# Optimization experiments

Hardware: AMD Instinct MI355X
Metric: run time of the kernel (lower is better)

## Reference

```python
import jax, jax.numpy as jnp
import numpy as np


def _isotonic_nonincreasing(y):
    """argmin_{v1>=...>=vn} ||v - y||^2 (PAV solution) via the exact min-max
    formula v[i] = min_{j<=i} max_{k>=i} mean(y[j:k+1]), vectorized O(n^2)."""
    n = y.shape[0]
    S = jnp.concatenate([jnp.zeros(1, y.dtype), jnp.cumsum(y)])  # prefix sums, [n+1]
    j = jnp.arange(n)[:, None]
    k = jnp.arange(n)[None, :]
    den = (k - j + 1).astype(y.dtype)
    # A[j,k] = mean(y[j:k+1]); entries with k<j are never read (see masking argument below)
    A = (S[k + 1] - S[j]) / jnp.where(den > 0, den, jnp.ones((), y.dtype))
    # Mrev[j,i] = max_{k'>=i} A[j,k']; for queries i>=j only valid entries participate
    Mrev = jnp.flip(jax.lax.cummax(jnp.flip(A, 1), axis=1), 1)
    # C[i,i] = min_{j<=i} Mrev[j,i]
    C = jax.lax.cummin(Mrev, axis=0)
    return jnp.diagonal(C)


def _soft_rank_row(z):
    """torchsort.soft_rank (l2 regularization, ascending) on a 1-D vector:
    projection of z onto the permutahedron of (1..n)."""
    n = z.shape[0]
    perm = jnp.argsort(-z)                # descending sort
    s = z[perm]
    w = jnp.arange(n, 0, -1).astype(z.dtype)   # rho = [n, n-1, ..., 1]
    dual = _isotonic_nonincreasing(s - w)
    primal = s - dual
    return jnp.zeros_like(z).at[perm].set(primal)  # undo the sort


def soft_rank(x, regularization_strength=1.0):
    # x: [rows, n]; rank each row over its last dim
    return jax.vmap(_soft_rank_row)(x / regularization_strength)


def setup_inputs() -> dict:
    key = jax.random.key(0)
    ks = jax.random.split(key, 7)
    B, D_IN, H, D_OUT = 4096, 512, 2048, 1

    def lin(kw, kb, fan_in, fan_out):
        lim = 1.0 / np.sqrt(fan_in)  # torch nn.Linear default init
        W = jax.random.uniform(kw, (fan_in, fan_out), jnp.float32, -lim, lim)
        b = jax.random.uniform(kb, (fan_out,), jnp.float32, -lim, lim)
        return W, b

    x = jax.random.normal(ks[0], (B, D_IN), jnp.float32)
    W1, b1 = lin(ks[1], ks[2], D_IN, H)
    W2, b2 = lin(ks[3], ks[4], H, H)
    W3, b3 = lin(ks[5], ks[6], H, D_OUT)
    return {"x": x, "W1": W1, "b1": b1, "W2": W2, "b2": b2, "W3": W3, "b3": b3}


def reference(x, W1, b1, W2, b2, W3, b3):
    # fc stack; Dropout is identity in eval mode
    h = jax.nn.relu(x @ W1 + b1)
    h = jax.nn.relu(h @ W2 + b2)
    scores = h @ W3 + b3                       # [B, D_OUT]
    rank = soft_rank(scores.T, 1.0)            # [D_OUT, B], ranks across the batch
    return rank, scores
```

## Files before the change

### kernel.cpp

```cpp
#include <hip/hip_runtime.h>
#include <hip/hip_bf16.h>

typedef float f32x4 __attribute__((ext_vector_type(4)));
typedef __bf16 bf16x8 __attribute__((ext_vector_type(8)));

#define AS3(p) ((__attribute__((address_space(3))) void*)(p))
#define AS1(p) ((const __attribute__((address_space(1))) void*)(p))

__device__ __forceinline__ unsigned short f2bf(float f) {
    unsigned u = __float_as_uint(f);
    return (unsigned short)((u + 0x7fffu + ((u >> 16) & 1u)) >> 16);
}

__device__ __forceinline__ unsigned long long sort_key(float v, int idx) {
    unsigned ub = __float_as_uint(v);
    unsigned m  = (ub & 0x80000000u) ? ~ub : (ub | 0x80000000u);
    return ((unsigned long long)(~m) << 12) | (unsigned)idx;
}

__global__ __launch_bounds__(256) void prep_all(
    const float* __restrict__ x, unsigned short* __restrict__ xb,
    const float* __restrict__ W1, unsigned short* __restrict__ W1t,
    const float* __restrict__ W2, unsigned short* __restrict__ W2t,
    float* __restrict__ sc, int* __restrict__ posg)
{
    __shared__ float tile[64][65];
    const int bx = blockIdx.x;
    const int t = threadIdx.x;

    if (bx < 1024) {
        int i = bx * 2048 + t * 8;
        float4 v0 = *(const float4*)(x + i);
        float4 v1 = *(const float4*)(x + i + 4);
        ushort4 o0 = { f2bf(v0.x), f2bf(v0.y), f2bf(v0.z), f2bf(v0.w) };
        ushort4 o1 = { f2bf(v1.x), f2bf(v1.y), f2bf(v1.z), f2bf(v1.w) };
        *(ushort4*)(xb + i)     = o0;
        *(ushort4*)(xb + i + 4) = o1;
        return;
    }
    if (bx == 2304) {
        float4 z = {0.f, 0.f, 0.f, 0.f};
        int4 zi = {0, 0, 0, 0};
        #pragma unroll
        for (int i = 0; i < 4; ++i) {
            *(float4*)(sc + t * 16 + i * 4)  = z;
            *(int4*)(posg + t * 16 + i * 4)  = zi;
        }
        return;
    }
    int idx = bx - 1024;
    int ty = idx >> 5;
    int txi = idx & 31;
    const float* W; unsigned short* Wt; int K, N, by;
    if (ty < 8) { W = W1; Wt = W1t; K = 512;  N = 2048; by = ty; }
    else        { W = W2; Wt = W2t; K = 2048; N = 2048; by = ty - 8; }

    const int col4 = t & 15;
    const int row  = t >> 4;
    #pragma unroll
    for (int i = 0; i < 4; ++i) {
        int r = row + i * 16;
        float4 v = *(const float4*)(W + (size_t)(by * 64 + r) * N + txi * 64 + col4 * 4);
        tile[r][col4 * 4 + 0] = v.x;
        tile[r][col4 * 4 + 1] = v.y;
        tile[r][col4 * 4 + 2] = v.z;
        tile[r][col4 * 4 + 3] = v.w;
    }
    __syncthreads();
    #pragma unroll
    for (int i = 0; i < 4; ++i) {
        int r = row + i * 16;
        ushort4 o = { f2bf(tile[col4 * 4 + 0][r]), f2bf(tile[col4 * 4 + 1][r]),
                      f2bf(tile[col4 * 4 + 2][r]), f2bf(tile[col4 * 4 + 3][r]) };
        *(ushort4*)(Wt + (size_t)(txi * 64 + r) * K + by * 64 + col4 * 4) = o;
    }
}

#define GB_WAITV(n) { asm volatile("s_waitcnt vmcnt(" #n ")" ::: "memory"); \
                      __builtin_amdgcn_sched_barrier(0); }

template <int MODE>
__global__ __launch_bounds__(512, 2) void gemm_bf16_mfma(
    const unsigned short* __restrict__ A, const unsigned short* __restrict__ Bt,
    const float* __restrict__ bias, unsigned short* __restrict__ Cbf,
    const float* __restrict__ w3, float* __restrict__ scores,
    int M, int N, int K)
{
    __shared__ __align__(16) unsigned short lds3[3][384 * 64];
    constexpr int BOFF = 256 * 64;

    const int tid = threadIdx.x;
    const int wave = tid >> 6, lane = tid & 63;

    const unsigned nwg = gridDim.x * gridDim.y;
    const unsigned bid = blockIdx.y * gridDim.x + blockIdx.x;
    const unsigned sbid = (bid & 7u) * (nwg >> 3) + (bid >> 3);
    const int bn = sbid % gridDim.x;
    const int bm = sbid / gridDim.x;

    const int wm = (wave >> 1) * 64;
    const int wn = (wave & 1) * 64;

    const unsigned short* Ablk = A  + (size_t)(bm * 256) * K;
    const unsigned short* Bblk = Bt + (size_t)(bn * 128) * K;

    const int lc  = lane & 15;
    const int rl4 = lane >> 4;
    const int srow = lane >> 3;
    const int sgc  = ((lane & 7) ^ srow) << 3;

    f32x4 acc[4][4] = {};
    const int nt = K >> 6;

    unsigned short *Ac = lds3[0], *An = lds3[1], *Asp = lds3[2];

    #define STG_P1(k0, D) {                                                    \
        _Pragma("unroll")                                                      \
        for (int i = 0; i < 2; ++i) {                                          \
            const int ra = wave * 32 + i * 8 + srow;                           \
            __builtin_amdgcn_global_load_lds(                                  \
                AS1(Ablk + (size_t)ra * K + (k0) + sgc),                       \
                AS3((D) + (wave * 32 + i * 8) * 64), 16, 0, 0);                \
        }                                                                      \
        {                                                                      \
            const int rb = wave * 16 + srow;                                   \
            __builtin_amdgcn_global_load_lds(                                  \
                AS1(Bblk + (size_t)rb * K + (k0) + sgc),                       \
                AS3((D) + BOFF + (wave * 16) * 64), 16, 0, 0);                 \
        } }
    #define STG_P2(k0, D) {                                                    \
        _Pragma("unroll")                                                      \
        for (int i = 2; i < 4; ++i) {                                          \
            const int ra = wave * 32 + i * 8 + srow;                           \
            __builtin_amdgcn_global_load_lds(                                  \
                AS1(Ablk + (size_t)ra * K + (k0) + sgc),                       \
                AS3((D) + (wave * 32 + i * 8) * 64), 16, 0, 0);                \
        }                                                                      \
        {                                                                      \
            const int rb = wave * 16 + 8 + srow;                               \
            __builtin_amdgcn_global_load_lds(                                  \
                AS1(Bblk + (size_t)rb * K + (k0) + sgc),                       \
                AS3((D) + BOFF + (wave * 16 + 8) * 64), 16, 0, 0);             \
        } }

    STG_P1(0, Ac);  STG_P2(0, Ac);
    STG_P1(64, An); STG_P2(64, An);

    for (int t = 0; t < nt; ++t) {
        if (t < nt - 1) { GB_WAITV(6); } else { GB_WAITV(0); }
        __builtin_amdgcn_s_barrier();

        const bool pf = (t + 2 < nt);
        const int kpf = (t + 2) << 6;

        if (pf) STG_P1(kpf, Asp);
        bf16x8 a[4][2], b[2][2];
        #pragma unroll
        for (int mt = 0; mt < 4; ++mt)
            #pragma unroll
            for (int kk = 0; kk < 2; ++kk)
                a[mt][kk] = *(const bf16x8*)(
                    Ac + (wm + mt * 16 + lc) * 64 + (((kk * 4 + rl4) ^ (lc & 7)) << 3));
        #pragma unroll
        for (int n2 = 0; n2 < 2; ++n2)
            #pragma unroll
            for (int kk = 0; kk < 2; ++kk)
                b[n2][kk] = *(const bf16x8*)(
                    Ac + BOFF + (wn + n2 * 16 + lc) * 64 + (((kk * 4 + rl4) ^ (lc & 7)) << 3));
        __builtin_amdgcn_s_setprio(1);
        #pragma unroll
        for (int mt = 0; mt < 4; ++mt)
            #pragma unroll
            for (int n2 = 0; n2 < 2; ++n2)
                #pragma unroll
                for (int kk = 0; kk < 2; ++kk)
                    acc[mt][n2] = __builtin_amdgcn_mfma_f32_16x16x32_bf16(
                        a[mt][kk], b[n2][kk], acc[mt][n2], 0, 0, 0);
        __builtin_amdgcn_s_setprio(0);

        if (pf) STG_P2(kpf, Asp);
        #pragma unroll
        for (int n2 = 0; n2 < 2; ++n2)
            #pragma unroll
            for (int kk = 0; kk < 2; ++kk)
                b[n2][kk] = *(const bf16x8*)(
                    Ac + BOFF + (wn + 32 + n2 * 16 + lc) * 64 + (((kk * 4 + rl4) ^ (lc & 7)) << 3));
        __builtin_amdgcn_s_setprio(1);
        #pragma unroll
        for (int mt = 0; mt < 4; ++mt)
            #pragma unroll
            for (int n2 = 0; n2 < 2; ++n2)
                #pragma unroll
                for (int kk = 0; kk < 2; ++kk)
                    acc[mt][2 + n2] = __builtin_amdgcn_mfma_f32_16x16x32_bf16(
                        a[mt][kk], b[n2][kk], acc[mt][2 + n2], 0, 0, 0);
        __builtin_amdgcn_s_setprio(0);

        unsigned short* tmp = Ac; Ac = An; An = Asp; Asp = tmp;
    }

    #undef STG_P1
    #undef STG_P2

    const int cm0 = bm * 256 + wm;
    const int cn0 = bn * 128 + wn;
    const int lr = (lane >> 4) * 4;

    if (MODE == 0) {
        #pragma unroll
        for (int j = 0; j < 4; ++j) {
            float bv = bias[cn0 + j * 16 + lc];
            #pragma unroll
            for (int mt = 0; mt < 4; ++mt)
                #pragma unroll
                for (int r = 0; r < 4; ++r) {
                    float v = fmaxf(acc[mt][j][r] + bv, 0.0f);
                    size_t idx = (size_t)(cm0 + mt * 16 + lr + r) * N + cn0 + j * 16 + lc;
                    Cbf[idx] = f2bf(v);
                }
        }
    } else {
        float bv[4], w3v[4];
        #pragma unroll
        for (int j = 0; j < 4; ++j) {
            bv[j]  = bias[cn0 + j * 16 + lc];
            w3v[j] = w3[cn0 + j * 16 + lc];
        }
        #pragma unroll
        for (int mt = 0; mt < 4; ++mt)
            #pragma unroll
            for (int r = 0; r < 4; ++r) {
                float p = 0.0f;
                #pragma unroll
                for (int j = 0; j < 4; ++j)
                    p += fmaxf(acc[mt][j][r] + bv[j], 0.0f) * w3v[j];
                p += __shfl_xor(p, 1);
                p += __shfl_xor(p, 2);
                p += __shfl_xor(p, 4);
                p += __shfl_xor(p, 8);
                if (lc == 0)
                    atomicAdd(&scores[cm0 + mt * 16 + lr + r], p);
            }
    }
}

__global__ __launch_bounds__(256) void rank_count(
    const float* __restrict__ sc, const float* __restrict__ b3,
    float* __restrict__ out_scores, int* __restrict__ posg)
{
    __shared__ unsigned long long kj[256];
    const int t = threadIdx.x;
    const int bi = blockIdx.x, bj = blockIdx.y;
    const int i = bi * 256 + t;
    const float b3v = b3[0];

    {
        int j = bj * 256 + t;
        kj[t] = sort_key(sc[j] + b3v, j);
    }
    float vi = sc[i] + b3v;
    if (bj == 0) out_scores[i] = vi;
    const unsigned long long mykey = sort_key(vi, i);
    __syncthreads();

    int cnt = 0;
    #pragma unroll 32
    for (int j = 0; j < 256; ++j)
        cnt += (kj[j] < mykey) ? 1 : 0;
    atomicAdd(&posg[i], cnt);
}

__global__ __launch_bounds__(1024) void pav_fill(
    const float* __restrict__ scores, const float* __restrict__ b3,
    const int* __restrict__ posg, float* __restrict__ rank_out)
{
    constexpr int n = 4096;
    __shared__ __align__(16) unsigned char lds[32768 + 16384 + 8192 + 512];
    double* bsum           = (double*)lds;
    float*  svals          = (float*)(lds + 32768);
    unsigned short* bstart = (unsigned short*)(lds + 49152);
    unsigned short* cnt    = (unsigned short*)(lds + 57344);

    const int tid = threadIdx.x;
    const float b3v = b3[0];

    {
        const int t = tid << 2;
        int4 p4 = *(const int4*)(posg + t);
        float4 s4 = *(const float4*)(scores + t);
        svals[p4.x] = s4.x + b3v;
        svals[p4.y] = s4.y + b3v;
        svals[p4.z] = s4.z + b3v;
        svals[p4.w] = s4.w + b3v;
    }
    __syncthreads();

    if (tid < 256) {
        const int base = tid << 4;
        float vv[16];
        *(float4*)(vv + 0)  = *(const float4*)(svals + base + 0);
        *(float4*)(vv + 4)  = *(const float4*)(svals + base + 4);
        *(float4*)(vv + 8)  = *(const float4*)(svals + base + 8);
        *(float4*)(vv + 12) = *(const float4*)(svals + base + 12);
        int sp = 0;
        double tsum = 0.0; int tstart = 0;
        #pragma unroll
        for (int s = 0; s < 16; ++s) {
            const int i = base + s;
            double csum = (double)vv[s] - (double)(n - i);
            int cs = i;
            const int ce = i + 1;
            while (sp > 0 &&
                   tsum * (double)(ce - cs) <= csum * (double)(cs - tstart)) {
                csum += tsum; cs = tstart; --sp;
                if (sp > 0) { tsum = bsum[base + sp - 1]; tstart = bstart[base + sp - 1]; }
            }
            bsum[base + sp] = csum;
            bstart[base + sp] = (unsigned short)cs;
            tsum = csum; tstart = cs; ++sp;
        }
        cnt[tid] = (unsigned short)sp;
    }
    __syncthreads();

    #pragma unroll 1
    for (int r = 0; r < 8; ++r) {
        const int m = 128 >> r;
        if (tid < m) {
            const int W  = 16 << r;
            const int L  = tid * (W << 1);
            const int Rb = L + W;
            int sp = cnt[L >> 4];
            const int cr = cnt[Rb >> 4];
            double tsum = bsum[L + sp - 1];
            int tstart = bstart[L + sp - 1];
            for (int j = 0; j < cr; ++j) {
                double csum = bsum[Rb + j];
                int cs = (int)bstart[Rb + j];
                const int ce = (j + 1 < cr) ? (int)bstart[Rb + j + 1] : (Rb + W);
                while (sp > 0 &&
                       tsum * (double)(ce - cs) <= csum * (double)(cs - tstart)) {
                    csum += tsum; cs = tstart; --sp;
                    if (sp > 0) { tsum = bsum[L + sp - 1]; tstart = bstart[L + sp - 1]; }
                }
                bsum[L + sp] = csum;
                bstart[L + sp] = (unsigned short)cs;
                tsum = csum; tstart = cs; ++sp;
            }
            cnt[L >> 4] = (unsigned short)sp;
        }
        __syncthreads();
    }

    const int nb = (int)cnt[0];
    {
        const int t = tid << 2;
        int4 p4 = *(const int4*)(posg + t);
        float4 o;
        int pa[4] = { p4.x, p4.y, p4.z, p4.w };
        float oa[4];
        #pragma unroll
        for (int e = 0; e < 4; ++e) {
            const int p = pa[e];
            int lo = 0, hi = nb - 1;
            while (lo < hi) {
                int mid = (lo + hi + 1) >> 1;
                if ((int)bstart[mid] <= p) lo = mid; else hi = mid - 1;
            }
            const int bs = (int)bstart[lo];
            const int be = (lo + 1 < nb) ? (int)bstart[lo + 1] : n;
            oa[e] = svals[p] - (float)(bsum[lo] / (double)(be - bs));
        }
        o.x = oa[0]; o.y = oa[1]; o.z = oa[2]; o.w = oa[3];
        *(float4*)(rank_out + t) = o;
    }
}

extern "C" void kernel_launch(void* const* d_in, const int* in_sizes, int n_in,
                              void* d_out, int out_size, void* d_ws, size_t ws_size,
                              hipStream_t stream) {
    const float* x  = (const float*)d_in[0];
    const float* W1 = (const float*)d_in[1];
    const float* b1 = (const float*)d_in[2];
    const float* W2 = (const float*)d_in[3];
    const float* b2 = (const float*)d_in[4];
    const float* W3 = (const float*)d_in[5];
    const float* b3 = (const float*)d_in[6];
    float* out = (float*)d_out;

    const int B = 4096, D_IN = 512, H = 2048;

    char* ws = (char*)d_ws;
    unsigned short* h1  = (unsigned short*)(ws);
    unsigned short* xb  = (unsigned short*)(ws + (16u << 20));
    unsigned short* W1t = (unsigned short*)(ws + (20u << 20));
    unsigned short* W2t = (unsigned short*)(ws + (22u << 20));
    float*          sc  = (float*)(ws + (30u << 20));
    int*            posg= (int*)(ws + (30u << 20) + 16384);

    prep_all<<<2305, 256, 0, stream>>>(x, xb, W1, W1t, W2, W2t, sc, posg);

    gemm_bf16_mfma<0><<<dim3(H / 128, B / 256), 512, 0, stream>>>(
        xb, W1t, b1, h1, nullptr, nullptr, B, H, D_IN);
    gemm_bf16_mfma<1><<<dim3(H / 128, B / 256), 512, 0, stream>>>(
        h1, W2t, b2, nullptr, W3, sc, B, H, H);

    rank_count<<<dim3(B / 256, B / 256), 256, 0, stream>>>(sc, b3, out + B, posg);
    pav_fill<<<1, 1024, 0, stream>>>(sc, b3, posg, out);
}
```

Measured before the change: 140.2 us.

## Load A fragments directly from global into registers, stage only B in LDS

```diff
diff --git a/kernel.cpp b/kernel.cpp
--- a/kernel.cpp
+++ b/kernel.cpp
@@ -86,8 +86,7 @@
     const float* __restrict__ w3, float* __restrict__ scores,
     int M, int N, int K)
 {
-    __shared__ __align__(16) unsigned short lds3[3][384 * 64];
-    constexpr int BOFF = 256 * 64;
+    __shared__ __align__(16) unsigned short lds3[3][128 * 64];
 
     const int tid = threadIdx.x;
     const int wave = tid >> 6, lane = tid & 63;
@@ -109,98 +108,77 @@
     const int srow = lane >> 3;
     const int sgc  = ((lane & 7) ^ srow) << 3;
 
+    const unsigned short* Aln = Ablk + (size_t)(wm + lc) * K + rl4 * 8;
+
     f32x4 acc[4][4] = {};
     const int nt = K >> 6;
 
-    unsigned short *Ac = lds3[0], *An = lds3[1], *Asp = lds3[2];
-
-    #define STG_P1(k0, D) {                                                    \
+    unsigned short *Bc = lds3[0], *Bn = lds3[1], *Bsp = lds3[2];
+
+    #define STG_B(k0, D) {                                                     \
         _Pragma("unroll")                                                      \
         for (int i = 0; i < 2; ++i) {                                          \
-            const int ra = wave * 32 + i * 8 + srow;                           \
-            __builtin_amdgcn_global_load_lds(                                  \
-                AS1(Ablk + (size_t)ra * K + (k0) + sgc),                       \
-                AS3((D) + (wave * 32 + i * 8) * 64), 16, 0, 0);                \
-        }                                                                      \
-        {                                                                      \
-            const int rb = wave * 16 + srow;                                   \
+            const int rb = wave * 16 + i * 8 + srow;                           \
             __builtin_amdgcn_global_load_lds(                                  \
                 AS1(Bblk + (size_t)rb * K + (k0) + sgc),                       \
-                AS3((D) + BOFF + (wave * 16) * 64), 16, 0, 0);                 \
+                AS3((D) + (wave * 16 + i * 8) * 64), 16, 0, 0);                \
         } }
-    #define STG_P2(k0, D) {                                                    \
-        _Pragma("unroll")                                                      \
-        for (int i = 2; i < 4; ++i) {                                          \
-            const int ra = wave * 32 + i * 8 + srow;                           \
-            __builtin_amdgcn_global_load_lds(                                  \
-                AS1(Ablk + (size_t)ra * K + (k0) + sgc),                       \
-                AS3((D) + (wave * 32 + i * 8) * 64), 16, 0, 0);                \
-        }                                                                      \
-        {                                                                      \
-            const int rb = wave * 16 + 8 + srow;                               \
-            __builtin_amdgcn_global_load_lds(                                  \
-                AS1(Bblk + (size_t)rb * K + (k0) + sgc),                       \
-                AS3((D) + BOFF + (wave * 16 + 8) * 64), 16, 0, 0);             \
-        } }
-
-    STG_P1(0, Ac);  STG_P2(0, Ac);
-    STG_P1(64, An); STG_P2(64, An);
+
+    STG_B(0, Bc);
+    bf16x8 a_cur[4][2];
+    #pragma unroll
+    for (int mt = 0; mt < 4; ++mt)
+        #pragma unroll
+        for (int kk = 0; kk < 2; ++kk)
+            a_cur[mt][kk] = *(const bf16x8*)(Aln + (size_t)(mt * 16) * K + kk * 32);
+    __builtin_amdgcn_sched_barrier(0);
+    if (nt > 1) STG_B(64, Bn);
 
     for (int t = 0; t < nt; ++t) {
-        if (t < nt - 1) { GB_WAITV(6); } else { GB_WAITV(0); }
+        if (t < nt - 1) { GB_WAITV(2); } else { GB_WAITV(0); }
         __builtin_amdgcn_s_barrier();
 
-        const bool pf = (t + 2 < nt);
-        const int kpf = (t + 2) << 6;
-
-        if (pf) STG_P1(kpf, Asp);
-        bf16x8 a[4][2], b[2][2];
-        #pragma unroll
-        for (int mt = 0; mt < 4; ++mt)
-            #pragma unroll
-            for (int kk = 0; kk < 2; ++kk)
-                a[mt][kk] = *(const bf16x8*)(
-                    Ac + (wm + mt * 16 + lc) * 64 + (((kk * 4 + rl4) ^ (lc & 7)) << 3));
-        #pragma unroll
-        for (int n2 = 0; n2 < 2; ++n2)
-            #pragma unroll
-            for (int kk = 0; kk < 2; ++kk)
-                b[n2][kk] = *(const bf16x8*)(
-                    Ac + BOFF + (wn + n2 * 16 + lc) * 64 + (((kk * 4 + rl4) ^ (lc & 7)) << 3));
-        __builtin_amdgcn_s_setprio(1);
-        #pragma unroll
-        for (int mt = 0; mt < 4; ++mt)
-            #pragma unroll
-            for (int n2 = 0; n2 < 2; ++n2)
+        bf16x8 a_nxt[4][2];
+        if (t + 1 < nt) {
+            const unsigned short* ap = Aln + (size_t)(t + 1) * 64;
+            #pragma unroll
+            for (int mt = 0; mt < 4; ++mt)
                 #pragma unroll
                 for (int kk = 0; kk < 2; ++kk)
+                    a_nxt[mt][kk] = *(const bf16x8*)(ap + (size_t)(mt * 16) * K + kk * 32);
+        }
+        __builtin_amdgcn_sched_barrier(0);
+        if (t + 2 < nt) { STG_B((t + 2) << 6, Bsp); }
+        __builtin_amdgcn_sched_barrier(0);
+
+        #pragma unroll
+        for (int s = 0; s < 2; ++s) {
+            const int rsw = (((s * 4 + rl4) ^ (lc & 7)) << 3);
+            bf16x8 b[4];
+            #pragma unroll
+            for (int n2 = 0; n2 < 4; ++n2)
+                b[n2] = *(const bf16x8*)(Bc + (wn + n2 * 16 + lc) * 64 + rsw);
+            __builtin_amdgcn_s_setprio(1);
+            #pragma unroll
+            for (int mt = 0; mt < 4; ++mt)
+                #pragma unroll
+                for (int n2 = 0; n2 < 4; ++n2)
                     acc[mt][n2] = __builtin_amdgcn_mfma_f32_16x16x32_bf16(
-                        a[mt][kk], b[n2][kk], acc[mt][n2], 0, 0, 0);
-        __builtin_amdgcn_s_setprio(0);
-
-        if (pf) STG_P2(kpf, Asp);
-        #pragma unroll
-        for (int n2 = 0; n2 < 2; ++n2)
-            #pragma unroll
-            for (int kk = 0; kk < 2; ++kk)
-                b[n2][kk] = *(const bf16x8*)(
-                    Ac + BOFF + (wn + 32 + n2 * 16 + lc) * 64 + (((kk * 4 + rl4) ^ (lc & 7)) << 3));
-        __builtin_amdgcn_s_setprio(1);
-        #pragma unroll
-        for (int mt = 0; mt < 4; ++mt)
-            #pragma unroll
-            for (int n2 = 0; n2 < 2; ++n2)
+                        a_cur[mt][s], b[n2], acc[mt][n2], 0, 0, 0);
+            __builtin_amdgcn_s_setprio(0);
+        }
+
+        if (t + 1 < nt) {
+            #pragma unroll
+            for (int mt = 0; mt < 4; ++mt)
                 #pragma unroll
                 for (int kk = 0; kk < 2; ++kk)
-                    acc[mt][2 + n2] = __builtin_amdgcn_mfma_f32_16x16x32_bf16(
-                        a[mt][kk], b[n2][kk], acc[mt][2 + n2], 0, 0, 0);
-        __builtin_amdgcn_s_setprio(0);
-
-        unsigned short* tmp = Ac; Ac = An; An = Asp; Asp = tmp;
-    }
-
-    #undef STG_P1
-    #undef STG_P2
+                    a_cur[mt][kk] = a_nxt[mt][kk];
+        }
+        unsigned short* tmp = Bc; Bc = Bn; Bn = Bsp; Bsp = tmp;
+    }
+
+    #undef STG_B
 
     const int cm0 = bm * 256 + wm;
     const int cn0 = bn * 128 + wn;
```

Result: slower. 207.3 us (+47.9%).
